# Kernel optimization log

Measured on AMD Instinct MI355X. Metric: run time of the kernel, lower is better.

Reference implementation:

```python
import jax, jax.numpy as jnp
import numpy as np

TIME_STEP = 0.02  # matches init_kwargs
B, T, D = 128, 2048, 4


def setup_inputs() -> dict:
    key = jax.random.key(0)
    k1, k2, k3, k4 = jax.random.split(key, 4)
    return {
        "h_real": jax.random.normal(k1, (B, T, D, D), dtype=jnp.float32),
        "h_imag": jax.random.normal(k2, (B, T, D, D), dtype=jnp.float32),
        "s_real": jax.random.normal(k3, (B, D, D), dtype=jnp.float32),
        "s_imag": jax.random.normal(k4, (B, D, D), dtype=jnp.float32),
    }


def reference(h_real, h_imag, s_real, s_imag):
    # dt = -1j * time_step (complex64 scalar, as in the keras cell)
    dt = jnp.asarray(-1j * TIME_STEP, dtype=jnp.complex64)
    H = (h_real + 1j * h_imag).astype(jnp.complex64)        # [B,T,D,D]
    state0 = (s_real + 1j * s_imag).astype(jnp.complex64)    # [B,D,D]
    Hs = jnp.transpose(H, (1, 0, 2, 3))                       # [T,B,D,D] for scan

    def step(state, h_t):
        # unitary = expm(-i*dt*H_t), batched over B via expm's leading-dim batching
        unitary = jax.scipy.linalg.expm(h_t * dt)             # [B,D,D]
        new_state = jnp.matmul(unitary, state)                # [B,D,D]
        return new_state, new_state

    _, seq = jax.lax.scan(step, state0, Hs)                   # seq: [T,B,D,D] complex64
    # return real/imag stacked so downstream harness sees a real tensor
    return jnp.stack([seq.real, seq.imag])                    # [2,T,B,D,D] float32
```

## Files before the change

### kernel.cpp

```cpp
#include <hip/hip_runtime.h>

namespace {

constexpr int    TT     = 2048;
constexpr int    BB     = 128;
constexpr int    CHUNK  = 8;
constexpr int    NCHUNK = TT / CHUNK;
constexpr float  DT     = 0.02f;
constexpr size_t HALF   = (size_t)TT * BB * 16;

__device__ __forceinline__ void cmm(const float* __restrict__ ar, const float* __restrict__ ai,
                                    const float* __restrict__ br, const float* __restrict__ bi,
                                    float* __restrict__ cr, float* __restrict__ ci) {
#pragma unroll
    for (int i = 0; i < 4; ++i) {
#pragma unroll
        for (int j = 0; j < 4; ++j) {
            float sr = 0.f, si = 0.f;
#pragma unroll
            for (int k = 0; k < 4; ++k) {
                const float xr = ar[i * 4 + k], xi = ai[i * 4 + k];
                const float yr = br[k * 4 + j], yi = bi[k * 4 + j];
                sr = fmaf(xr, yr, sr);
                sr = fmaf(-xi, yi, sr);
                si = fmaf(xr, yi, si);
                si = fmaf(xi, yr, si);
            }
            cr[i * 4 + j] = sr;
            ci[i * 4 + j] = si;
        }
    }
}

__device__ __forceinline__ unsigned int pack2(float a, float b) {
    return (__float_as_uint(a) >> 16) | (__float_as_uint(b) & 0xFFFF0000u);
}
__device__ __forceinline__ float unlo(unsigned int u) { return __uint_as_float(u << 16); }
__device__ __forceinline__ float unhi(unsigned int u) { return __uint_as_float(u & 0xFFFF0000u); }

}

__global__ __launch_bounds__(256) void kA_expm_scan(const float* __restrict__ hr,
                                                    const float* __restrict__ hi,
                                                    uint4* __restrict__ L,
                                                    float* __restrict__ totals) {
    const int gid  = blockIdx.x * 256 + threadIdx.x;
    const int b    = gid >> 11;
    const int t    = gid & (TT - 1);
    const int sub  = t & (CHUNK - 1);
    const int c    = t >> 3;
    const int lane = threadIdx.x & 63;

    float a_r[16], a_i[16];
    {
        const float4* p4r = reinterpret_cast<const float4*>(hr) + (size_t)gid * 4;
        const float4* p4i = reinterpret_cast<const float4*>(hi) + (size_t)gid * 4;
#pragma unroll
        for (int v = 0; v < 4; ++v) {
            const float4 rr = p4r[v];
            const float4 im = p4i[v];
            a_r[v * 4 + 0] = DT * im.x;  a_i[v * 4 + 0] = -DT * rr.x;
            a_r[v * 4 + 1] = DT * im.y;  a_i[v * 4 + 1] = -DT * rr.y;
            a_r[v * 4 + 2] = DT * im.z;  a_i[v * 4 + 2] = -DT * rr.z;
            a_r[v * 4 + 3] = DT * im.w;  a_i[v * 4 + 3] = -DT * rr.w;
        }
    }

    float er[16], ei[16];
    {
        float a2r[16], a2i[16];
        cmm(a_r, a_i, a_r, a_i, a2r, a2i);
        float tr[16], ti[16];
#pragma unroll
        for (int e = 0; e < 16; ++e) {
            const float d = (e % 5 == 0) ? 1.0f : 0.0f;
            tr[e] = fmaf(a_r[e], 1.f / 6.f, d * 0.5f);
            tr[e] = fmaf(a2r[e], 1.f / 24.f, tr[e]);
            ti[e] = a_i[e] * (1.f / 6.f);
            ti[e] = fmaf(a2i[e], 1.f / 24.f, ti[e]);
        }
        cmm(a2r, a2i, tr, ti, er, ei);
#pragma unroll
        for (int e = 0; e < 16; ++e) {
            const float d = (e % 5 == 0) ? 1.0f : 0.0f;
            er[e] = er[e] + d + a_r[e];
            ei[e] = ei[e] + a_i[e];
        }
    }

#pragma unroll
    for (int d = 1; d < CHUNK; d <<= 1) {
        int src = lane - d;
        if (src < 0) src = 0;
        float qr[16], qi[16];
#pragma unroll
        for (int e = 0; e < 16; ++e) {
            qr[e] = __shfl(er[e], src, 64);
            qi[e] = __shfl(ei[e], src, 64);
        }
        float nr[16], ni[16];
        cmm(er, ei, qr, qi, nr, ni);
        const bool pred = (sub >= d);
#pragma unroll
        for (int e = 0; e < 16; ++e) {
            er[e] = pred ? nr[e] : er[e];
            ei[e] = pred ? ni[e] : ei[e];
        }
    }

    if (sub == CHUNK - 1) {
        float* tp = totals + ((size_t)b * NCHUNK + c) * 32;
#pragma unroll
        for (int e = 0; e < 16; ++e) {
            tp[e]      = er[e];
            tp[16 + e] = ei[e];
        }
    }

    {
        uint4 w0, w1, w2, w3;
        w0.x = pack2(er[0],  er[1]);   w0.y = pack2(er[2],  er[3]);
        w0.z = pack2(er[4],  er[5]);   w0.w = pack2(er[6],  er[7]);
        w1.x = pack2(er[8],  er[9]);   w1.y = pack2(er[10], er[11]);
        w1.z = pack2(er[12], er[13]);  w1.w = pack2(er[14], er[15]);
        w2.x = pack2(ei[0],  ei[1]);   w2.y = pack2(ei[2],  ei[3]);
        w2.z = pack2(ei[4],  ei[5]);   w2.w = pack2(ei[6],  ei[7]);
        w3.x = pack2(ei[8],  ei[9]);   w3.y = pack2(ei[10], ei[11]);
        w3.z = pack2(ei[12], ei[13]);  w3.w = pack2(ei[14], ei[15]);
        uint4* Lp = L + (size_t)gid * 4;
        Lp[0] = w0; Lp[1] = w1; Lp[2] = w2; Lp[3] = w3;
    }
}

__global__ __launch_bounds__(256) void kC_carry(const float* __restrict__ totals,
                                                const float* __restrict__ sr,
                                                const float* __restrict__ si,
                                                float* __restrict__ carry) {
    __shared__ float sRe[16][NCHUNK];
    __shared__ float sIm[16][NCHUNK];

    const int ct = threadIdx.x;
    const int b  = blockIdx.x;

    float pr[16], pi[16];
    if (ct == 0) {
#pragma unroll
        for (int e = 0; e < 16; ++e) {
            pr[e] = sr[b * 16 + e];
            pi[e] = si[b * 16 + e];
        }
    } else {
        const float* tp = totals + ((size_t)b * NCHUNK + ct - 1) * 32;
#pragma unroll
        for (int e = 0; e < 16; ++e) {
            pr[e] = tp[e];
            pi[e] = tp[16 + e];
        }
    }

#pragma unroll
    for (int e = 0; e < 16; ++e) {
        sRe[e][ct] = pr[e];
        sIm[e][ct] = pi[e];
    }
    __syncthreads();

#pragma unroll
    for (int d = 1; d < NCHUNK; d <<= 1) {
        if (ct >= d) {
            float qr[16], qi[16];
#pragma unroll
            for (int e = 0; e < 16; ++e) {
                qr[e] = sRe[e][ct - d];
                qi[e] = sIm[e][ct - d];
            }
            float nr[16], ni[16];
            cmm(pr, pi, qr, qi, nr, ni);
#pragma unroll
            for (int e = 0; e < 16; ++e) {
                pr[e] = nr[e];
                pi[e] = ni[e];
            }
        }
        __syncthreads();
        if (ct >= d) {
#pragma unroll
            for (int e = 0; e < 16; ++e) {
                sRe[e][ct] = pr[e];
                sIm[e][ct] = pi[e];
            }
        }
        __syncthreads();
    }

    float* cp = carry + ((size_t)b * NCHUNK + ct) * 32;
#pragma unroll
    for (int e = 0; e < 16; ++e) {
        cp[e]      = pr[e];
        cp[16 + e] = pi[e];
    }
}

__global__ __launch_bounds__(256) void kD_final(const uint4* __restrict__ L,
                                                const float* __restrict__ carry,
                                                float* __restrict__ out) {
    __shared__ float lds[32 * 16 * 17];

    const int bid   = blockIdx.x;
    const int tileT = bid & 127;
    const int tileB = bid >> 7;
    const int t0 = tileT * 16, b0 = tileB * 16;
    const int tid = threadIdx.x;

    {
        const int bloc = tid >> 4, tloc = tid & 15;
        const int tt = t0 + tloc;
        const size_t gi = ((size_t)(b0 + bloc) * TT + tt);

        const uint4* Lp = L + gi * 4;
        const uint4 w0 = Lp[0], w1 = Lp[1], w2 = Lp[2], w3 = Lp[3];
        float l_r[16], l_i[16];
        l_r[0]  = unlo(w0.x); l_r[1]  = unhi(w0.x); l_r[2]  = unlo(w0.y); l_r[3]  = unhi(w0.y);
        l_r[4]  = unlo(w0.z); l_r[5]  = unhi(w0.z); l_r[6]  = unlo(w0.w); l_r[7]  = unhi(w0.w);
        l_r[8]  = unlo(w1.x); l_r[9]  = unhi(w1.x); l_r[10] = unlo(w1.y); l_r[11] = unhi(w1.y);
        l_r[12] = unlo(w1.z); l_r[13] = unhi(w1.z); l_r[14] = unlo(w1.w); l_r[15] = unhi(w1.w);
        l_i[0]  = unlo(w2.x); l_i[1]  = unhi(w2.x); l_i[2]  = unlo(w2.y); l_i[3]  = unhi(w2.y);
        l_i[4]  = unlo(w2.z); l_i[5]  = unhi(w2.z); l_i[6]  = unlo(w2.w); l_i[7]  = unhi(w2.w);
        l_i[8]  = unlo(w3.x); l_i[9]  = unhi(w3.x); l_i[10] = unlo(w3.y); l_i[11] = unhi(w3.y);
        l_i[12] = unlo(w3.z); l_i[13] = unhi(w3.z); l_i[14] = unlo(w3.w); l_i[15] = unhi(w3.w);

        float c_r[16], c_i[16];
        const float* cp = carry + ((size_t)(b0 + bloc) * NCHUNK + (tt >> 3)) * 32;
#pragma unroll
        for (int e = 0; e < 16; ++e) {
            c_r[e] = cp[e];
            c_i[e] = cp[16 + e];
        }

        float o_r[16], o_i[16];
        cmm(l_r, l_i, c_r, c_i, o_r, o_i);

        const int slot = bloc * 17 + tloc;
#pragma unroll
        for (int e = 0; e < 16; ++e) {
            lds[e * 272 + slot]        = o_r[e];
            lds[(e + 16) * 272 + slot] = o_i[e];
        }
    }
    __syncthreads();

    {
        const int u = tid >> 4;
        const int v = tid & 15;
        const int slot = v * 17 + u;

        float r2[16], i2[16];
#pragma unroll
        for (int e = 0; e < 16; ++e) {
            r2[e] = lds[e * 272 + slot];
            i2[e] = lds[(e + 16) * 272 + slot];
        }

        const size_t oi = ((size_t)(t0 + u) * BB + (b0 + v)) * 16;
        float4* orp = reinterpret_cast<float4*>(out + oi);
        float4* oip = reinterpret_cast<float4*>(out + HALF + oi);
#pragma unroll
        for (int w = 0; w < 4; ++w) {
            orp[w] = make_float4(r2[w * 4 + 0], r2[w * 4 + 1], r2[w * 4 + 2], r2[w * 4 + 3]);
            oip[w] = make_float4(i2[w * 4 + 0], i2[w * 4 + 1], i2[w * 4 + 2], i2[w * 4 + 3]);
        }
    }
}

extern "C" void kernel_launch(void* const* d_in, const int* in_sizes, int n_in,
                              void* d_out, int out_size, void* d_ws, size_t ws_size,
                              hipStream_t stream) {
    const float* hr = (const float*)d_in[0];
    const float* hi = (const float*)d_in[1];
    const float* sr = (const float*)d_in[2];
    const float* si = (const float*)d_in[3];
    float* out    = (float*)d_out;
    float* totals = (float*)d_ws;
    float* carry  = (float*)d_ws + (size_t)BB * NCHUNK * 32;
    uint4* L      = (uint4*)((float*)d_ws + 2 * (size_t)BB * NCHUNK * 32);

    kA_expm_scan<<<(BB * TT) / 256, 256, 0, stream>>>(hr, hi, L, totals);
    kC_carry    <<<BB, 256, 0, stream>>>(totals, sr, si, carry);
    kD_final    <<<(BB * TT) / 256, 256, 0, stream>>>(L, carry, out);
}
```

Measured before the change: 127.1 us.

## Fuse three kernels into one persistent kernel with software grid barriers

Merges the expm/chunk-scan, carry-scan and final-apply kernels into a single launch. Two atomic-counter grid barriers separate the phases, and each thread keeps its packed local prefix in registers instead of writing it to and reading it back from global memory. This removes that intermediate traffic and two launch gaps. The cost is a tiny init kernel, a spin wait, and the requirement that all 1024 blocks be co-resident (launch_bounds 256,4); otherwise the kernel deadlocks. The totals and carry accesses are also vectorised to float4.

```diff
diff --git a/kernel.cpp b/kernel.cpp
--- a/kernel.cpp
+++ b/kernel.cpp
@@ -8,6 +8,7 @@
 constexpr int    NCHUNK = TT / CHUNK;
 constexpr float  DT     = 0.02f;
 constexpr size_t HALF   = (size_t)TT * BB * 16;
+constexpr int    NBLK   = (BB * TT) / 256;
 
 __device__ __forceinline__ void cmm(const float* __restrict__ ar, const float* __restrict__ ai,
                                     const float* __restrict__ br, const float* __restrict__ bi,
@@ -32,29 +33,79 @@
     }
 }
 
+__device__ __forceinline__ void cmm_acc(const float* __restrict__ ar, const float* __restrict__ ai,
+                                        const float* __restrict__ br, const float* __restrict__ bi,
+                                        float* __restrict__ cr, float* __restrict__ ci) {
+#pragma unroll
+    for (int i = 0; i < 4; ++i) {
+#pragma unroll
+        for (int j = 0; j < 4; ++j) {
+            float sr = cr[i * 4 + j], si = ci[i * 4 + j];
+#pragma unroll
+            for (int k = 0; k < 4; ++k) {
+                const float xr = ar[i * 4 + k], xi = ai[i * 4 + k];
+                const float yr = br[k * 4 + j], yi = bi[k * 4 + j];
+                sr = fmaf(xr, yr, sr);
+                sr = fmaf(-xi, yi, sr);
+                si = fmaf(xr, yi, si);
+                si = fmaf(xi, yr, si);
+            }
+            cr[i * 4 + j] = sr;
+            ci[i * 4 + j] = si;
+        }
+    }
+}
+
 __device__ __forceinline__ unsigned int pack2(float a, float b) {
     return (__float_as_uint(a) >> 16) | (__float_as_uint(b) & 0xFFFF0000u);
 }
 __device__ __forceinline__ float unlo(unsigned int u) { return __uint_as_float(u << 16); }
 __device__ __forceinline__ float unhi(unsigned int u) { return __uint_as_float(u & 0xFFFF0000u); }
 
-}
-
-__global__ __launch_bounds__(256) void kA_expm_scan(const float* __restrict__ hr,
-                                                    const float* __restrict__ hi,
-                                                    uint4* __restrict__ L,
-                                                    float* __restrict__ totals) {
-    const int gid  = blockIdx.x * 256 + threadIdx.x;
-    const int b    = gid >> 11;
-    const int t    = gid & (TT - 1);
-    const int sub  = t & (CHUNK - 1);
-    const int c    = t >> 3;
-    const int lane = threadIdx.x & 63;
-
-    float a_r[16], a_i[16];
+__device__ __forceinline__ void gsync(unsigned int* cnt) {
+    __syncthreads();
+    if (threadIdx.x == 0) {
+        __threadfence();
+        __hip_atomic_fetch_add(cnt, 1u, __ATOMIC_ACQ_REL, __HIP_MEMORY_SCOPE_AGENT);
+        while (__hip_atomic_load(cnt, __ATOMIC_ACQUIRE, __HIP_MEMORY_SCOPE_AGENT) <
+               (unsigned int)NBLK) {
+            __builtin_amdgcn_s_sleep(1);
+        }
+    }
+    __syncthreads();
+}
+
+}
+
+__global__ void k_init(unsigned int* bar) {
+    bar[0] = 0u;
+    bar[1] = 0u;
+}
+
+__global__ __launch_bounds__(256, 4) void k_fused(
+        const float* __restrict__ hr, const float* __restrict__ hi,
+        const float* __restrict__ sr, const float* __restrict__ si,
+        float* __restrict__ out, float* __restrict__ totals,
+        float* __restrict__ carry, unsigned int* __restrict__ bar) {
+    __shared__ float scratch[32 * 272];
+
+    const int tid   = threadIdx.x;
+    const int bid   = blockIdx.x;
+    const int tileT = bid & 127;
+    const int tileB = bid >> 7;
+    const int t0 = tileT * 16, b0 = tileB * 16;
+    const int bloc = tid >> 4, tloc = tid & 15;
+    const int lane = tid & 63;
+    const int sub  = tloc & 7;
+    const int b = b0 + bloc;
+    const int t = t0 + tloc;
+
+    float er[16], ei[16];
     {
-        const float4* p4r = reinterpret_cast<const float4*>(hr) + (size_t)gid * 4;
-        const float4* p4i = reinterpret_cast<const float4*>(hi) + (size_t)gid * 4;
+        float a_r[16], a_i[16];
+        const size_t gi = (size_t)b * TT + t;
+        const float4* p4r = reinterpret_cast<const float4*>(hr) + gi * 4;
+        const float4* p4i = reinterpret_cast<const float4*>(hi) + gi * 4;
 #pragma unroll
         for (int v = 0; v < 4; ++v) {
             const float4 rr = p4r[v];
@@ -64,28 +115,21 @@
             a_r[v * 4 + 2] = DT * im.z;  a_i[v * 4 + 2] = -DT * rr.z;
             a_r[v * 4 + 3] = DT * im.w;  a_i[v * 4 + 3] = -DT * rr.w;
         }
-    }
-
-    float er[16], ei[16];
-    {
+
         float a2r[16], a2i[16];
         cmm(a_r, a_i, a_r, a_i, a2r, a2i);
-        float tr[16], ti[16];
+        float t6r[16], t6i[16];
 #pragma unroll
         for (int e = 0; e < 16; ++e) {
             const float d = (e % 5 == 0) ? 1.0f : 0.0f;
-            tr[e] = fmaf(a_r[e], 1.f / 6.f, d * 0.5f);
-            tr[e] = fmaf(a2r[e], 1.f / 24.f, tr[e]);
-            ti[e] = a_i[e] * (1.f / 6.f);
-            ti[e] = fmaf(a2i[e], 1.f / 24.f, ti[e]);
-        }
-        cmm(a2r, a2i, tr, ti, er, ei);
-#pragma unroll
-        for (int e = 0; e < 16; ++e) {
-            const float d = (e % 5 == 0) ? 1.0f : 0.0f;
-            er[e] = er[e] + d + a_r[e];
-            ei[e] = ei[e] + a_i[e];
-        }
+            t6r[e] = fmaf(a_r[e], 1.f / 6.f, d * 0.5f);
+            t6r[e] = fmaf(a2r[e], 1.f / 24.f, t6r[e]);
+            t6i[e] = a_i[e] * (1.f / 6.f);
+            t6i[e] = fmaf(a2i[e], 1.f / 24.f, t6i[e]);
+            er[e]  = a_r[e] + d;
+            ei[e]  = a_i[e];
+        }
+        cmm_acc(a2r, a2i, t6r, t6i, er, ei);
     }
 
 #pragma unroll
@@ -109,132 +153,112 @@
     }
 
     if (sub == CHUNK - 1) {
-        float* tp = totals + ((size_t)b * NCHUNK + c) * 32;
-#pragma unroll
-        for (int e = 0; e < 16; ++e) {
-            tp[e]      = er[e];
-            tp[16 + e] = ei[e];
-        }
-    }
+        float4* tp = reinterpret_cast<float4*>(totals + ((size_t)b * NCHUNK + (t >> 3)) * 32);
+        tp[0] = make_float4(er[0],  er[1],  er[2],  er[3]);
+        tp[1] = make_float4(er[4],  er[5],  er[6],  er[7]);
+        tp[2] = make_float4(er[8],  er[9],  er[10], er[11]);
+        tp[3] = make_float4(er[12], er[13], er[14], er[15]);
+        tp[4] = make_float4(ei[0],  ei[1],  ei[2],  ei[3]);
+        tp[5] = make_float4(ei[4],  ei[5],  ei[6],  ei[7]);
+        tp[6] = make_float4(ei[8],  ei[9],  ei[10], ei[11]);
+        tp[7] = make_float4(ei[12], ei[13], ei[14], ei[15]);
+    }
+
+    unsigned int Lp[16];
+#pragma unroll
+    for (int k = 0; k < 8; ++k) {
+        Lp[k]     = pack2(er[2 * k], er[2 * k + 1]);
+        Lp[8 + k] = pack2(ei[2 * k], ei[2 * k + 1]);
+    }
+
+    gsync(bar + 0);
+
+    if (bid < BB) {
+        float* sRe = scratch;
+        float* sIm = scratch + 16 * NCHUNK;
+        const int ct = tid;
+
+        float pr[16], pi[16];
+        if (ct == 0) {
+            const float4* s4r = reinterpret_cast<const float4*>(sr) + bid * 4;
+            const float4* s4i = reinterpret_cast<const float4*>(si) + bid * 4;
+#pragma unroll
+            for (int q = 0; q < 4; ++q) {
+                const float4 xr = s4r[q], xi = s4i[q];
+                pr[q * 4 + 0] = xr.x; pr[q * 4 + 1] = xr.y; pr[q * 4 + 2] = xr.z; pr[q * 4 + 3] = xr.w;
+                pi[q * 4 + 0] = xi.x; pi[q * 4 + 1] = xi.y; pi[q * 4 + 2] = xi.z; pi[q * 4 + 3] = xi.w;
+            }
+        } else {
+            const float4* tp = reinterpret_cast<const float4*>(
+                totals + ((size_t)bid * NCHUNK + ct - 1) * 32);
+#pragma unroll
+            for (int q = 0; q < 4; ++q) {
+                const float4 xr = tp[q], xi = tp[4 + q];
+                pr[q * 4 + 0] = xr.x; pr[q * 4 + 1] = xr.y; pr[q * 4 + 2] = xr.z; pr[q * 4 + 3] = xr.w;
+                pi[q * 4 + 0] = xi.x; pi[q * 4 + 1] = xi.y; pi[q * 4 + 2] = xi.z; pi[q * 4 + 3] = xi.w;
+            }
+        }
+
+#pragma unroll
+        for (int e = 0; e < 16; ++e) {
+            sRe[e * NCHUNK + ct] = pr[e];
+            sIm[e * NCHUNK + ct] = pi[e];
+        }
+        __syncthreads();
+
+        for (int d = 1; d < NCHUNK; d <<= 1) {
+            if (ct >= d) {
+                float qr[16], qi[16];
+#pragma unroll
+                for (int e = 0; e < 16; ++e) {
+                    qr[e] = sRe[e * NCHUNK + ct - d];
+                    qi[e] = sIm[e * NCHUNK + ct - d];
+                }
+                float nr[16], ni[16];
+                cmm(pr, pi, qr, qi, nr, ni);
+#pragma unroll
+                for (int e = 0; e < 16; ++e) { pr[e] = nr[e]; pi[e] = ni[e]; }
+            }
+            __syncthreads();
+            if (ct >= d) {
+#pragma unroll
+                for (int e = 0; e < 16; ++e) {
+                    sRe[e * NCHUNK + ct] = pr[e];
+                    sIm[e * NCHUNK + ct] = pi[e];
+                }
+            }
+            __syncthreads();
+        }
+
+        float4* cp = reinterpret_cast<float4*>(carry + ((size_t)bid * NCHUNK + ct) * 32);
+        cp[0] = make_float4(pr[0],  pr[1],  pr[2],  pr[3]);
+        cp[1] = make_float4(pr[4],  pr[5],  pr[6],  pr[7]);
+        cp[2] = make_float4(pr[8],  pr[9],  pr[10], pr[11]);
+        cp[3] = make_float4(pr[12], pr[13], pr[14], pr[15]);
+        cp[4] = make_float4(pi[0],  pi[1],  pi[2],  pi[3]);
+        cp[5] = make_float4(pi[4],  pi[5],  pi[6],  pi[7]);
+        cp[6] = make_float4(pi[8],  pi[9],  pi[10], pi[11]);
+        cp[7] = make_float4(pi[12], pi[13], pi[14], pi[15]);
+    }
+
+    gsync(bar + 1);
 
     {
-        uint4 w0, w1, w2, w3;
-        w0.x = pack2(er[0],  er[1]);   w0.y = pack2(er[2],  er[3]);
-        w0.z = pack2(er[4],  er[5]);   w0.w = pack2(er[6],  er[7]);
-        w1.x = pack2(er[8],  er[9]);   w1.y = pack2(er[10], er[11]);
-        w1.z = pack2(er[12], er[13]);  w1.w = pack2(er[14], er[15]);
-        w2.x = pack2(ei[0],  ei[1]);   w2.y = pack2(ei[2],  ei[3]);
-        w2.z = pack2(ei[4],  ei[5]);   w2.w = pack2(ei[6],  ei[7]);
-        w3.x = pack2(ei[8],  ei[9]);   w3.y = pack2(ei[10], ei[11]);
-        w3.z = pack2(ei[12], ei[13]);  w3.w = pack2(ei[14], ei[15]);
-        uint4* Lp = L + (size_t)gid * 4;
-        Lp[0] = w0; Lp[1] = w1; Lp[2] = w2; Lp[3] = w3;
-    }
-}
-
-__global__ __launch_bounds__(256) void kC_carry(const float* __restrict__ totals,
-                                                const float* __restrict__ sr,
-                                                const float* __restrict__ si,
-                                                float* __restrict__ carry) {
-    __shared__ float sRe[16][NCHUNK];
-    __shared__ float sIm[16][NCHUNK];
-
-    const int ct = threadIdx.x;
-    const int b  = blockIdx.x;
-
-    float pr[16], pi[16];
-    if (ct == 0) {
-#pragma unroll
-        for (int e = 0; e < 16; ++e) {
-            pr[e] = sr[b * 16 + e];
-            pi[e] = si[b * 16 + e];
-        }
-    } else {
-        const float* tp = totals + ((size_t)b * NCHUNK + ct - 1) * 32;
-#pragma unroll
-        for (int e = 0; e < 16; ++e) {
-            pr[e] = tp[e];
-            pi[e] = tp[16 + e];
-        }
-    }
-
-#pragma unroll
-    for (int e = 0; e < 16; ++e) {
-        sRe[e][ct] = pr[e];
-        sIm[e][ct] = pi[e];
-    }
-    __syncthreads();
-
-#pragma unroll
-    for (int d = 1; d < NCHUNK; d <<= 1) {
-        if (ct >= d) {
-            float qr[16], qi[16];
-#pragma unroll
-            for (int e = 0; e < 16; ++e) {
-                qr[e] = sRe[e][ct - d];
-                qi[e] = sIm[e][ct - d];
-            }
-            float nr[16], ni[16];
-            cmm(pr, pi, qr, qi, nr, ni);
-#pragma unroll
-            for (int e = 0; e < 16; ++e) {
-                pr[e] = nr[e];
-                pi[e] = ni[e];
-            }
-        }
-        __syncthreads();
-        if (ct >= d) {
-#pragma unroll
-            for (int e = 0; e < 16; ++e) {
-                sRe[e][ct] = pr[e];
-                sIm[e][ct] = pi[e];
-            }
-        }
-        __syncthreads();
-    }
-
-    float* cp = carry + ((size_t)b * NCHUNK + ct) * 32;
-#pragma unroll
-    for (int e = 0; e < 16; ++e) {
-        cp[e]      = pr[e];
-        cp[16 + e] = pi[e];
-    }
-}
-
-__global__ __launch_bounds__(256) void kD_final(const uint4* __restrict__ L,
-                                                const float* __restrict__ carry,
-                                                float* __restrict__ out) {
-    __shared__ float lds[32 * 16 * 17];
-
-    const int bid   = blockIdx.x;
-    const int tileT = bid & 127;
-    const int tileB = bid >> 7;
-    const int t0 = tileT * 16, b0 = tileB * 16;
-    const int tid = threadIdx.x;
-
-    {
-        const int bloc = tid >> 4, tloc = tid & 15;
-        const int tt = t0 + tloc;
-        const size_t gi = ((size_t)(b0 + bloc) * TT + tt);
-
-        const uint4* Lp = L + gi * 4;
-        const uint4 w0 = Lp[0], w1 = Lp[1], w2 = Lp[2], w3 = Lp[3];
         float l_r[16], l_i[16];
-        l_r[0]  = unlo(w0.x); l_r[1]  = unhi(w0.x); l_r[2]  = unlo(w0.y); l_r[3]  = unhi(w0.y);
-        l_r[4]  = unlo(w0.z); l_r[5]  = unhi(w0.z); l_r[6]  = unlo(w0.w); l_r[7]  = unhi(w0.w);
-        l_r[8]  = unlo(w1.x); l_r[9]  = unhi(w1.x); l_r[10] = unlo(w1.y); l_r[11] = unhi(w1.y);
-        l_r[12] = unlo(w1.z); l_r[13] = unhi(w1.z); l_r[14] = unlo(w1.w); l_r[15] = unhi(w1.w);
-        l_i[0]  = unlo(w2.x); l_i[1]  = unhi(w2.x); l_i[2]  = unlo(w2.y); l_i[3]  = unhi(w2.y);
-        l_i[4]  = unlo(w2.z); l_i[5]  = unhi(w2.z); l_i[6]  = unlo(w2.w); l_i[7]  = unhi(w2.w);
-        l_i[8]  = unlo(w3.x); l_i[9]  = unhi(w3.x); l_i[10] = unlo(w3.y); l_i[11] = unhi(w3.y);
-        l_i[12] = unlo(w3.z); l_i[13] = unhi(w3.z); l_i[14] = unlo(w3.w); l_i[15] = unhi(w3.w);
+#pragma unroll
+        for (int k = 0; k < 8; ++k) {
+            l_r[2 * k] = unlo(Lp[k]);     l_r[2 * k + 1] = unhi(Lp[k]);
+            l_i[2 * k] = unlo(Lp[8 + k]); l_i[2 * k + 1] = unhi(Lp[8 + k]);
+        }
 
         float c_r[16], c_i[16];
-        const float* cp = carry + ((size_t)(b0 + bloc) * NCHUNK + (tt >> 3)) * 32;
-#pragma unroll
-        for (int e = 0; e < 16; ++e) {
-            c_r[e] = cp[e];
-            c_i[e] = cp[16 + e];
+        const float4* cp = reinterpret_cast<const float4*>(
+            carry + ((size_t)b * NCHUNK + (t >> 3)) * 32);
+#pragma unroll
+        for (int q = 0; q < 4; ++q) {
+            const float4 xr = cp[q], xi = cp[4 + q];
+            c_r[q * 4 + 0] = xr.x; c_r[q * 4 + 1] = xr.y; c_r[q * 4 + 2] = xr.z; c_r[q * 4 + 3] = xr.w;
+            c_i[q * 4 + 0] = xi.x; c_i[q * 4 + 1] = xi.y; c_i[q * 4 + 2] = xi.z; c_i[q * 4 + 3] = xi.w;
         }
 
         float o_r[16], o_i[16];
@@ -243,12 +267,11 @@
         const int slot = bloc * 17 + tloc;
 #pragma unroll
         for (int e = 0; e < 16; ++e) {
-            lds[e * 272 + slot]        = o_r[e];
-            lds[(e + 16) * 272 + slot] = o_i[e];
+            scratch[e * 272 + slot]        = o_r[e];
+            scratch[(e + 16) * 272 + slot] = o_i[e];
         }
     }
     __syncthreads();
-
     {
         const int u = tid >> 4;
         const int v = tid & 15;
@@ -257,8 +280,8 @@
         float r2[16], i2[16];
 #pragma unroll
         for (int e = 0; e < 16; ++e) {
-            r2[e] = lds[e * 272 + slot];
-            i2[e] = lds[(e + 16) * 272 + slot];
+            r2[e] = scratch[e * 272 + slot];
+            i2[e] = scratch[(e + 16) * 272 + slot];
         }
 
         const size_t oi = ((size_t)(t0 + u) * BB + (b0 + v)) * 16;
@@ -282,9 +305,8 @@
     float* out    = (float*)d_out;
     float* totals = (float*)d_ws;
     float* carry  = (float*)d_ws + (size_t)BB * NCHUNK * 32;
-    uint4* L      = (uint4*)((float*)d_ws + 2 * (size_t)BB * NCHUNK * 32);
-
-    kA_expm_scan<<<(BB * TT) / 256, 256, 0, stream>>>(hr, hi, L, totals);
-    kC_carry    <<<BB, 256, 0, stream>>>(totals, sr, si, carry);
-    kD_final    <<<(BB * TT) / 256, 256, 0, stream>>>(L, carry, out);
-}
+    unsigned int* bar = (unsigned int*)((float*)d_ws + 2 * (size_t)BB * NCHUNK * 32);
+
+    k_init <<<1, 1, 0, stream>>>(bar);
+    k_fused<<<NBLK, 256, 0, stream>>>(hr, hi, sr, si, out, totals, carry, bar);
+}
```

After: 442.6 us. 3.48x slower.
